# Performance work log

Measured on AMD Instinct MI355X. Metric: run time of the kernel, lower is better.

The kernel has to match this reference:

```python
import jax, jax.numpy as jnp
import numpy as np

EPS = 1e-3  # Keras BatchNormalization default epsilon
ROWS = 14


def _lstm_step(h, c, x, W, U, b, act):
    # Keras gate order: i, f, g(cell), o
    z = x @ W + h @ U + b
    i, f, g, o = jnp.split(z, 4, axis=-1)
    c = jax.nn.sigmoid(f) * c + jax.nn.sigmoid(i) * act(g)
    h = jax.nn.sigmoid(o) * act(c)
    return h, c


def _lstm(xs, W, U, b, act):
    # xs: [B, T, F] -> (last_h, last_c), zero initial state
    B = xs.shape[0]
    D = U.shape[0]
    h0 = jnp.zeros((B, D), xs.dtype)
    c0 = jnp.zeros((B, D), xs.dtype)

    def step(carry, x):
        h, c = _lstm_step(carry[0], carry[1], x, W, U, b, act)
        return (h, c), h

    (h, c), hs = jax.lax.scan(step, (h0, c0), jnp.swapaxes(xs, 0, 1))
    return jnp.swapaxes(hs, 0, 1), h, c


def _bn(x, gamma, beta):
    # training-mode batchnorm over all axes but the last (channel) axis
    axes = tuple(range(x.ndim - 1))
    mean = jnp.mean(x, axis=axes)
    var = jnp.var(x, axis=axes)
    return (x - mean) * jax.lax.rsqrt(var + EPS) * gamma + beta


def setup_inputs() -> dict:
    key = jax.random.key(0)
    B, T, F = 65536, 32, 16
    D = 8   # lstm_forward_dims = output_dims * 2
    Do = 4  # lstm_backward_dims = output_dims
    ks = jax.random.split(key, 10)
    p = lambda k, shp: (0.1 * jax.random.normal(k, shp)).astype(jnp.float32)
    return {
        "noise_seed": jax.random.normal(ks[0], (B, T, F), dtype=jnp.float32),
        "W0": p(ks[1], (F, 4 * D)), "U0": p(ks[2], (D, 4 * D)), "b0": jnp.zeros((4 * D,), jnp.float32),
        "gamma_h": jnp.ones((D,), jnp.float32), "beta_h": jnp.zeros((D,), jnp.float32),
        "gamma_c": jnp.ones((D,), jnp.float32), "beta_c": jnp.zeros((D,), jnp.float32),
        "W1": p(ks[3], (D, 4 * D)), "U1": p(ks[4], (D, 4 * D)), "b1": jnp.zeros((4 * D,), jnp.float32),
        "gamma3": jnp.ones((D,), jnp.float32), "beta3": jnp.zeros((D,), jnp.float32),
        "W2": p(ks[5], (D, 4 * Do)), "U2": p(ks[6], (Do, 4 * Do)), "b2": jnp.zeros((4 * Do,), jnp.float32),
        "training": 1,
    }


def reference(noise_seed, W0, U0, b0, gamma_h, beta_h, gamma_c, beta_c,
              W1, U1, b1, gamma3, beta3, W2, U2, b2, training):
    # init LSTM (tanh activation), keep final states
    _, h, c = _lstm(noise_seed, W0, U0, b0, jnp.tanh)
    h = _bn(h, gamma_h, beta_h)
    c = _bn(c, gamma_c, beta_c)

    def step(carry, _):
        h, c = carry
        h2, c2 = _lstm_step(h, c, h, W1, U1, b1, jax.nn.relu)
        return (h2, c2), h2

    _, hs = jax.lax.scan(step, (h, c), None, length=ROWS)  # [ROWS, B, D]
    bars = jnp.swapaxes(hs[::-1], 0, 1)                    # reversed, [B, ROWS, D]
    bars = _bn(bars, gamma3, beta3)

    # backward LSTM (relu activation), return_sequences
    out, _, _ = _lstm(bars, W2, U2, b2, jax.nn.relu)       # [B, ROWS, Do]
    return out
```

## Files before the change

### kernel.cpp

```cpp
#include <hip/hip_runtime.h>
#include <hip/hip_bf16.h>

#define EPSV 1e-3f

__device__ __forceinline__ float rcp_fast(float x){ return __builtin_amdgcn_rcpf(x); }
__device__ __forceinline__ float sigm(float x){ return rcp_fast(1.f + __expf(-x)); }
__device__ __forceinline__ float tanh_fast(float x){
    float e = __expf(2.f * x);
    return 1.f - 2.f * rcp_fast(e + 1.f);
}

template<int K>
__device__ __forceinline__ float bc8(float v){
    return __int_as_float(__builtin_amdgcn_ds_swizzle(__float_as_int(v), (K << 5) | 0x18));
}
#define BC8_ALL(dst, src) do { \
    dst[0]=bc8<0>(src); dst[1]=bc8<1>(src); dst[2]=bc8<2>(src); dst[3]=bc8<3>(src); \
    dst[4]=bc8<4>(src); dst[5]=bc8<5>(src); dst[6]=bc8<6>(src); dst[7]=bc8<7>(src); } while(0)

__global__ __launch_bounds__(256) void k1_lstm0(
    const float* __restrict__ noise, const float* __restrict__ W0,
    const float* __restrict__ U0, const float* __restrict__ b0,
    float* __restrict__ Hbuf, float* __restrict__ Cbuf, double* __restrict__ stats1)
{
    __shared__ float lw[8*68];
    __shared__ float lu[8*36];
    __shared__ float red[4][4][8];

    const int tid = threadIdx.x;
    const int d = tid & 7;
    {
        const int i0 = tid;
        const int dd0 = i0 & 7, fg0 = i0 >> 3, f0 = fg0 >> 2, g0 = fg0 & 3;
        lw[dd0*68 + fg0] = W0[f0*32 + 8*g0 + dd0];
        const int i1 = tid + 256;
        const int dd1 = i1 & 7, fg1 = i1 >> 3, f1 = fg1 >> 2, g1 = fg1 & 3;
        lw[dd1*68 + fg1] = W0[f1*32 + 8*g1 + dd1];
    }
    {
        const int dd = tid & 7, eg = tid >> 3, e = eg >> 2, g = eg & 3;
        lu[dd*36 + eg] = U0[e*32 + 8*g + dd];
    }
    float b0v[4];
    #pragma unroll
    for (int g = 0; g < 4; ++g) b0v[g] = b0[8*g + d];
    __syncthreads();

    const float* wp = &lw[d*68];
    const float* up = &lu[d*36];
    const size_t b = (size_t)blockIdx.x * 32 + (tid >> 3);
    const float4* __restrict__ xrow = reinterpret_cast<const float4*>(noise + b * 512);

    float h = 0.f, c = 0.f;
    float4 q0 = xrow[0], q1 = xrow[1], q2 = xrow[2], q3 = xrow[3];
    #pragma unroll 2
    for (int t = 0; t < 32; ++t){
        const float x[16] = {q0.x,q0.y,q0.z,q0.w, q1.x,q1.y,q1.z,q1.w,
                             q2.x,q2.y,q2.z,q2.w, q3.x,q3.y,q3.z,q3.w};
        const int tn = (t + 1) & 31;
        q0 = xrow[tn*4+0]; q1 = xrow[tn*4+1]; q2 = xrow[tn*4+2]; q3 = xrow[tn*4+3];
        float hall[8]; BC8_ALL(hall, h);
        float z0 = b0v[0], z1 = b0v[1], z2 = b0v[2], z3 = b0v[3];
        #pragma unroll
        for (int f = 0; f < 16; ++f){
            const float4 w = *reinterpret_cast<const float4*>(wp + f*4);
            z0 = fmaf(x[f], w.x, z0); z1 = fmaf(x[f], w.y, z1);
            z2 = fmaf(x[f], w.z, z2); z3 = fmaf(x[f], w.w, z3);
        }
        #pragma unroll
        for (int e = 0; e < 8; ++e){
            const float4 u = *reinterpret_cast<const float4*>(up + e*4);
            z0 = fmaf(hall[e], u.x, z0); z1 = fmaf(hall[e], u.y, z1);
            z2 = fmaf(hall[e], u.z, z2); z3 = fmaf(hall[e], u.w, z3);
        }
        c = fmaf(sigm(z1), c, sigm(z0) * tanh_fast(z2));
        h = sigm(z3) * tanh_fast(c);
    }
    Hbuf[(size_t)blockIdx.x*256 + tid] = h;
    Cbuf[(size_t)blockIdx.x*256 + tid] = c;

    float v0 = h, v1 = h*h, v2 = c, v3 = c*c;
    v0 += __shfl_down(v0,32); v0 += __shfl_down(v0,16); v0 += __shfl_down(v0,8);
    v1 += __shfl_down(v1,32); v1 += __shfl_down(v1,16); v1 += __shfl_down(v1,8);
    v2 += __shfl_down(v2,32); v2 += __shfl_down(v2,16); v2 += __shfl_down(v2,8);
    v3 += __shfl_down(v3,32); v3 += __shfl_down(v3,16); v3 += __shfl_down(v3,8);
    const int w = tid >> 6;
    if ((tid & 63) < 8){ red[0][w][d]=v0; red[1][w][d]=v1; red[2][w][d]=v2; red[3][w][d]=v3; }
    __syncthreads();
    if (tid < 32){
        const int s = tid >> 3, dd = tid & 7;
        float acc = red[s][0][dd] + red[s][1][dd] + red[s][2][dd] + red[s][3][dd];
        atomicAdd(stats1 + s*8 + dd, (double)acc);
    }
}

__global__ __launch_bounds__(256) void k2_ar(
    const float* __restrict__ Hbuf, const float* __restrict__ Cbuf,
    const double* __restrict__ stats1,
    const float* __restrict__ gamma_h, const float* __restrict__ beta_h,
    const float* __restrict__ gamma_c, const float* __restrict__ beta_c,
    const float* __restrict__ W1, const float* __restrict__ U1, const float* __restrict__ b1,
    double* __restrict__ stats3, int B)
{
    __shared__ float ls[8*36];
    __shared__ float red[2][4][8];
    const int tid = threadIdx.x;
    const int d = tid & 7;
    {
        const int dd = tid & 7, eg = tid >> 3, e = eg >> 2, g = eg & 3;
        ls[dd*36 + eg] = W1[e*32 + 8*g + dd] + U1[e*32 + 8*g + dd];
    }
    const double invB = 1.0 / (double)B;
    const float meanH = (float)(stats1[d]      * invB);
    const float eH2   = (float)(stats1[8 + d]  * invB);
    const float meanC = (float)(stats1[16 + d] * invB);
    const float eC2   = (float)(stats1[24 + d] * invB);
    const float aH = gamma_h[d] * rsqrtf(eH2 - meanH*meanH + EPSV);
    const float aC = gamma_c[d] * rsqrtf(eC2 - meanC*meanC + EPSV);
    float h = fmaf(Hbuf[(size_t)blockIdx.x*256 + tid], aH, beta_h[d] - meanH*aH);
    float c = fmaf(Cbuf[(size_t)blockIdx.x*256 + tid], aC, beta_c[d] - meanC*aC);
    float bcv[4];
    #pragma unroll
    for (int g = 0; g < 4; ++g) bcv[g] = b1[8*g + d];
    __syncthreads();
    const float* sp = &ls[d*36];

    float s1 = 0.f, s2 = 0.f;
    #pragma unroll
    for (int r = 0; r < 14; ++r){
        float hall[8]; BC8_ALL(hall, h);
        float z0 = bcv[0], z1 = bcv[1], z2 = bcv[2], z3 = bcv[3];
        #pragma unroll
        for (int e = 0; e < 8; ++e){
            const float4 u = *reinterpret_cast<const float4*>(sp + e*4);
            z0 = fmaf(hall[e], u.x, z0); z1 = fmaf(hall[e], u.y, z1);
            z2 = fmaf(hall[e], u.z, z2); z3 = fmaf(hall[e], u.w, z3);
        }
        c = fmaf(sigm(z1), c, sigm(z0) * fmaxf(z2, 0.f));
        h = sigm(z3) * fmaxf(c, 0.f);
        s1 += h; s2 = fmaf(h, h, s2);
    }
    s1 += __shfl_down(s1,32); s1 += __shfl_down(s1,16); s1 += __shfl_down(s1,8);
    s2 += __shfl_down(s2,32); s2 += __shfl_down(s2,16); s2 += __shfl_down(s2,8);
    const int w = tid >> 6;
    if ((tid & 63) < 8){ red[0][w][d] = s1; red[1][w][d] = s2; }
    __syncthreads();
    if (tid < 16){
        const int s = tid >> 3, dd = tid & 7;
        float acc = red[s][0][dd] + red[s][1][dd] + red[s][2][dd] + red[s][3][dd];
        atomicAdd(stats3 + s*8 + dd, (double)acc);
    }
}

__global__ __launch_bounds__(256) void k3_out(
    const float* __restrict__ Hbuf, const float* __restrict__ Cbuf,
    const double* __restrict__ stats1, const double* __restrict__ stats3,
    const float* __restrict__ gamma_h, const float* __restrict__ beta_h,
    const float* __restrict__ gamma_c, const float* __restrict__ beta_c,
    const float* __restrict__ W1, const float* __restrict__ U1, const float* __restrict__ b1,
    const float* __restrict__ gamma3, const float* __restrict__ beta3,
    const float* __restrict__ W2, const float* __restrict__ U2, const float* __restrict__ b2,
    float* __restrict__ out, int B)
{
    __shared__ float ls[8*36];
    __shared__ float lw2[4*36];
    __shared__ float lu2[4*20];
    const int tid = threadIdx.x;
    const int d = tid & 7;
    {
        const int dd = tid & 7, eg = tid >> 3, e = eg >> 2, g = eg & 3;
        ls[dd*36 + eg] = W1[e*32 + 8*g + dd] + U1[e*32 + 8*g + dd];
    }
    if (tid < 128){
        const int qq = tid & 3, eg = tid >> 2, e = eg >> 2, g = eg & 3;
        lw2[qq*36 + eg] = W2[e*16 + 4*g + qq];
    }
    if (tid < 64){
        const int qq = tid & 3, eg = tid >> 2, e = eg >> 2, g = eg & 3;
        lu2[qq*20 + eg] = U2[e*16 + 4*g + qq];
    }
    const double invB = 1.0 / (double)B;
    const float meanH = (float)(stats1[d]      * invB);
    const float eH2   = (float)(stats1[8 + d]  * invB);
    const float meanC = (float)(stats1[16 + d] * invB);
    const float eC2   = (float)(stats1[24 + d] * invB);
    const float aH = gamma_h[d] * rsqrtf(eH2 - meanH*meanH + EPSV);
    const float aC = gamma_c[d] * rsqrtf(eC2 - meanC*meanC + EPSV);
    float h = fmaf(Hbuf[(size_t)blockIdx.x*256 + tid], aH, beta_h[d] - meanH*aH);
    float c = fmaf(Cbuf[(size_t)blockIdx.x*256 + tid], aC, beta_c[d] - meanC*aC);
    float bcv[4];
    #pragma unroll
    for (int g = 0; g < 4; ++g) bcv[g] = b1[8*g + d];
    __syncthreads();
    const float* sp = &ls[d*36];

    float barh[14];
    #pragma unroll
    for (int r = 0; r < 14; ++r){
        float hall[8]; BC8_ALL(hall, h);
        float z0 = bcv[0], z1 = bcv[1], z2 = bcv[2], z3 = bcv[3];
        #pragma unroll
        for (int e = 0; e < 8; ++e){
            const float4 u = *reinterpret_cast<const float4*>(sp + e*4);
            z0 = fmaf(hall[e], u.x, z0); z1 = fmaf(hall[e], u.y, z1);
            z2 = fmaf(hall[e], u.z, z2); z3 = fmaf(hall[e], u.w, z3);
        }
        c = fmaf(sigm(z1), c, sigm(z0) * fmaxf(z2, 0.f));
        h = sigm(z3) * fmaxf(c, 0.f);
        barh[r] = h;
    }
    const double invN = 1.0 / ((double)B * 14.0);
    const float mean3 = (float)(stats3[d]     * invN);
    const float e32   = (float)(stats3[8 + d] * invN);
    const float a3 = gamma3[d] * rsqrtf(e32 - mean3*mean3 + EPSV);
    const float b3 = beta3[d] - mean3*a3;
    #pragma unroll
    for (int r = 0; r < 14; ++r) barh[r] = fmaf(barh[r], a3, b3);

    const int q = d & 3;
    const float* w2p = &lw2[q*36];
    const float* u2p = &lu2[q*20];
    float b2v[4];
    #pragma unroll
    for (int g = 0; g < 4; ++g) b2v[g] = b2[4*g + q];

    float ho = 0.f, co = 0.f;
    const size_t obase = ((size_t)blockIdx.x*32 + (tid >> 3)) * 56;
    #pragma unroll
    for (int r = 0; r < 14; ++r){
        const float cur = barh[13 - r];
        float be[8]; BC8_ALL(be, cur);
        float h4[4];
        h4[0]=bc8<0>(ho); h4[1]=bc8<1>(ho); h4[2]=bc8<2>(ho); h4[3]=bc8<3>(ho);
        float z0 = b2v[0], z1 = b2v[1], z2 = b2v[2], z3 = b2v[3];
        #pragma unroll
        for (int e = 0; e < 8; ++e){
            const float4 w = *reinterpret_cast<const float4*>(w2p + e*4);
            z0 = fmaf(be[e], w.x, z0); z1 = fmaf(be[e], w.y, z1);
            z2 = fmaf(be[e], w.z, z2); z3 = fmaf(be[e], w.w, z3);
        }
        #pragma unroll
        for (int e = 0; e < 4; ++e){
            const float4 u = *reinterpret_cast<const float4*>(u2p + e*4);
            z0 = fmaf(h4[e], u.x, z0); z1 = fmaf(h4[e], u.y, z1);
            z2 = fmaf(h4[e], u.z, z2); z3 = fmaf(h4[e], u.w, z3);
        }
        co = fmaf(sigm(z1), co, sigm(z0) * fmaxf(z2, 0.f));
        ho = sigm(z3) * fmaxf(co, 0.f);
        if (d < 4) out[obase + r*4 + d] = ho;
    }
}

extern "C" void kernel_launch(void* const* d_in, const int* in_sizes, int n_in,
                              void* d_out, int out_size, void* d_ws, size_t ws_size,
                              hipStream_t stream)
{
    const float* noise   = (const float*)d_in[0];
    const float* W0      = (const float*)d_in[1];
    const float* U0      = (const float*)d_in[2];
    const float* b0      = (const float*)d_in[3];
    const float* gamma_h = (const float*)d_in[4];
    const float* beta_h  = (const float*)d_in[5];
    const float* gamma_c = (const float*)d_in[6];
    const float* beta_c  = (const float*)d_in[7];
    const float* W1      = (const float*)d_in[8];
    const float* U1      = (const float*)d_in[9];
    const float* b1      = (const float*)d_in[10];
    const float* gamma3  = (const float*)d_in[11];
    const float* beta3   = (const float*)d_in[12];
    const float* W2      = (const float*)d_in[13];
    const float* U2      = (const float*)d_in[14];
    const float* b2      = (const float*)d_in[15];

    const int B = in_sizes[0] / (32 * 16);
    double* stats1 = (double*)d_ws;
    double* stats3 = stats1 + 32;
    float* Hbuf = (float*)((char*)d_ws + 512);
    float* Cbuf = Hbuf + (size_t)B * 8;

    hipMemsetAsync(d_ws, 0, 48 * sizeof(double), stream);
    const int nb = B / 32;
    k1_lstm0<<<nb, 256, 0, stream>>>(noise, W0, U0, b0, Hbuf, Cbuf, stats1);
    k2_ar<<<nb, 256, 0, stream>>>(Hbuf, Cbuf, stats1, gamma_h, beta_h, gamma_c, beta_c,
                                  W1, U1, b1, stats3, B);
    k3_out<<<nb, 256, 0, stream>>>(Hbuf, Cbuf, stats1, stats3, gamma_h, beta_h, gamma_c, beta_c,
                                   W1, U1, b1, gamma3, beta3, W2, U2, b2, (float*)d_out, B);
}
```

Baseline: 158.6 us.

## Precompute LSTM0 input projections in double-buffered LDS chunks overlapping the recurrence

The first LSTM kernel now computes the input projection x@W0 (+bias) separately. Each thread owns one gate column and writes results for 4 timesteps of 4 samples into a double-buffered shared-memory z buffer. The recurrent loop then reads precomputed gate pre-activations and applies only the h@U0 part, while the next chunk's projection is computed ahead of it. The aim is to take the 16-wide input matmul off the serial dependency chain and load noise with coalesced per-column reads. In exchange it uses about 34KB of extra LDS, adds a block barrier per chunk, and sets waves_per_eu hints that may lower occupancy.

```diff
diff --git a/kernel.cpp b/kernel.cpp
--- a/kernel.cpp
+++ b/kernel.cpp
@@ -18,64 +18,96 @@
     dst[0]=bc8<0>(src); dst[1]=bc8<1>(src); dst[2]=bc8<2>(src); dst[3]=bc8<3>(src); \
     dst[4]=bc8<4>(src); dst[5]=bc8<5>(src); dst[6]=bc8<6>(src); dst[7]=bc8<7>(src); } while(0)
 
-__global__ __launch_bounds__(256) void k1_lstm0(
+__global__ __launch_bounds__(256)
+__attribute__((amdgpu_waves_per_eu(1, 4)))
+void k1_lstm0(
     const float* __restrict__ noise, const float* __restrict__ W0,
     const float* __restrict__ U0, const float* __restrict__ b0,
     float* __restrict__ Hbuf, float* __restrict__ Cbuf, double* __restrict__ stats1)
 {
-    __shared__ float lw[8*68];
-    __shared__ float lu[8*36];
+    __shared__ float wbuf[16*33];
+    __shared__ float ubufT[8*36];
+    __shared__ float bbuf[32];
+    __shared__ float zbuf[2][32*132];
     __shared__ float red[4][4][8];
 
     const int tid = threadIdx.x;
-    const int d = tid & 7;
     {
-        const int i0 = tid;
-        const int dd0 = i0 & 7, fg0 = i0 >> 3, f0 = fg0 >> 2, g0 = fg0 & 3;
-        lw[dd0*68 + fg0] = W0[f0*32 + 8*g0 + dd0];
-        const int i1 = tid + 256;
-        const int dd1 = i1 & 7, fg1 = i1 >> 3, f1 = fg1 >> 2, g1 = fg1 & 3;
-        lw[dd1*68 + fg1] = W0[f1*32 + 8*g1 + dd1];
-    }
-    {
+        const int i0 = tid,        f0 = i0 >> 5, c0 = i0 & 31;
+        const int i1 = tid + 256,  f1 = i1 >> 5, c1 = i1 & 31;
+        wbuf[f0*33 + c0] = W0[f0*32 + c0];
+        wbuf[f1*33 + c1] = W0[f1*32 + c1];
         const int dd = tid & 7, eg = tid >> 3, e = eg >> 2, g = eg & 3;
-        lu[dd*36 + eg] = U0[e*32 + 8*g + dd];
-    }
-    float b0v[4];
-    #pragma unroll
-    for (int g = 0; g < 4; ++g) b0v[g] = b0[8*g + d];
-    __syncthreads();
-
-    const float* wp = &lw[d*68];
-    const float* up = &lu[d*36];
-    const size_t b = (size_t)blockIdx.x * 32 + (tid >> 3);
-    const float4* __restrict__ xrow = reinterpret_cast<const float4*>(noise + b * 512);
-
-    float h = 0.f, c = 0.f;
-    float4 q0 = xrow[0], q1 = xrow[1], q2 = xrow[2], q3 = xrow[3];
-    #pragma unroll 2
-    for (int t = 0; t < 32; ++t){
-        const float x[16] = {q0.x,q0.y,q0.z,q0.w, q1.x,q1.y,q1.z,q1.w,
-                             q2.x,q2.y,q2.z,q2.w, q3.x,q3.y,q3.z,q3.w};
-        const int tn = (t + 1) & 31;
-        q0 = xrow[tn*4+0]; q1 = xrow[tn*4+1]; q2 = xrow[tn*4+2]; q3 = xrow[tn*4+3];
-        float hall[8]; BC8_ALL(hall, h);
-        float z0 = b0v[0], z1 = b0v[1], z2 = b0v[2], z3 = b0v[3];
-        #pragma unroll
-        for (int f = 0; f < 16; ++f){
-            const float4 w = *reinterpret_cast<const float4*>(wp + f*4);
-            z0 = fmaf(x[f], w.x, z0); z1 = fmaf(x[f], w.y, z1);
-            z2 = fmaf(x[f], w.z, z2); z3 = fmaf(x[f], w.w, z3);
-        }
-        #pragma unroll
-        for (int e = 0; e < 8; ++e){
-            const float4 u = *reinterpret_cast<const float4*>(up + e*4);
-            z0 = fmaf(hall[e], u.x, z0); z1 = fmaf(hall[e], u.y, z1);
-            z2 = fmaf(hall[e], u.z, z2); z3 = fmaf(hall[e], u.w, z3);
-        }
-        c = fmaf(sigm(z1), c, sigm(z0) * tanh_fast(z2));
-        h = sigm(z3) * tanh_fast(c);
-    }
+        ubufT[dd*36 + eg] = U0[e*32 + 8*g + dd];
+        if (tid < 32) bbuf[tid] = b0[tid];
+    }
+    __syncthreads();
+
+    const int col = tid & 31;
+    const int j   = tid >> 5;
+    const int d   = tid & 7;
+    const int sB  = tid >> 3;
+    const size_t sampleBase = (size_t)blockIdx.x * 32;
+
+    float wcol[16];
+    #pragma unroll
+    for (int f = 0; f < 16; ++f) wcol[f] = wbuf[f*33 + col];
+    const float bcol = bbuf[col];
+    float4 uq[8];
+    #pragma unroll
+    for (int e = 0; e < 8; ++e) uq[e] = *reinterpret_cast<const float4*>(&ubufT[d*36 + e*4]);
+
+#define PHASE_A(CK, BUF) do {                                                     \
+    _Pragma("unroll 1")                                                           \
+    for (int k = 0; k < 4; ++k){                                                  \
+        const int sl = k*8 + j;                                                   \
+        const float4* xp = reinterpret_cast<const float4*>(                       \
+            noise + (sampleBase + sl)*512 + (CK)*64);                             \
+        float* zw = &zbuf[BUF][sl*132 + col];                                     \
+        _Pragma("unroll")                                                         \
+        for (int tp = 0; tp < 4; ++tp){                                           \
+            float4 q0 = xp[tp*4+0], q1 = xp[tp*4+1], q2 = xp[tp*4+2], q3 = xp[tp*4+3]; \
+            float z = bcol;                                                       \
+            z = fmaf(q0.x, wcol[0], z);  z = fmaf(q0.y, wcol[1], z);              \
+            z = fmaf(q0.z, wcol[2], z);  z = fmaf(q0.w, wcol[3], z);              \
+            z = fmaf(q1.x, wcol[4], z);  z = fmaf(q1.y, wcol[5], z);              \
+            z = fmaf(q1.z, wcol[6], z);  z = fmaf(q1.w, wcol[7], z);              \
+            z = fmaf(q2.x, wcol[8], z);  z = fmaf(q2.y, wcol[9], z);              \
+            z = fmaf(q2.z, wcol[10], z); z = fmaf(q2.w, wcol[11], z);             \
+            z = fmaf(q3.x, wcol[12], z); z = fmaf(q3.y, wcol[13], z);             \
+            z = fmaf(q3.z, wcol[14], z); z = fmaf(q3.w, wcol[15], z);             \
+            zw[tp*33] = z;                                                        \
+        }                                                                         \
+    }                                                                             \
+} while(0)
+
+    float h = 0.f, c = 0.f, hall[8];
+    #pragma unroll
+    for (int e = 0; e < 8; ++e) hall[e] = 0.f;
+
+    PHASE_A(0, 0);
+    __syncthreads();
+
+    #pragma unroll 1
+    for (int ck = 0; ck < 8; ++ck){
+        if (ck < 7) PHASE_A(ck + 1, (ck + 1) & 1);
+        const float* zs = &zbuf[ck & 1][sB*132 + d];
+        #pragma unroll
+        for (int tp = 0; tp < 4; ++tp){
+            float z0 = zs[tp*33], z1 = zs[tp*33 + 8], z2 = zs[tp*33 + 16], z3 = zs[tp*33 + 24];
+            #pragma unroll
+            for (int e = 0; e < 8; ++e){
+                z0 = fmaf(hall[e], uq[e].x, z0); z1 = fmaf(hall[e], uq[e].y, z1);
+                z2 = fmaf(hall[e], uq[e].z, z2); z3 = fmaf(hall[e], uq[e].w, z3);
+            }
+            c = fmaf(sigm(z1), c, sigm(z0) * tanh_fast(z2));
+            h = sigm(z3) * tanh_fast(c);
+            BC8_ALL(hall, h);
+        }
+        __syncthreads();
+    }
+#undef PHASE_A
+
     Hbuf[(size_t)blockIdx.x*256 + tid] = h;
     Cbuf[(size_t)blockIdx.x*256 + tid] = c;
 
```

After: 208.0 us. 1.31x slower.
